# Optimization experiments

Hardware: AMD Instinct MI355X
Metric: run time of the kernel (lower is better)

Reference implementation:

```python
import jax, jax.numpy as jnp
import numpy as np

BATCH = 2048
N_MOL = 16
HEADS = 8      # C
A_DIM = 64     # embedding_dim
B_DIM = 64     # output_dim
D_IN = 64
POS_DIM = 6
CA = HEADS * A_DIM
CB = HEADS * B_DIM


def _pos_encoding(n_mol):
    # get_pos_encoding_(pos, C=6, dim_embedding=3): 3 sin + 3 cos terms
    def enc(p):
        return np.array([np.sin(p / 6.0 ** (2 * i / 3.0)) for i in (1, 2, 3)]
                        + [np.cos(p / 6.0 ** (2 * i / 3.0)) for i in (1, 2, 3)])
    return np.stack([enc(i) for i in range(n_mol)]).astype(np.float32)  # (n_mol, 6)


def setup_inputs() -> dict:
    key = jax.random.key(0)
    ks = jax.random.split(key, 8)
    d_ext = D_IN + POS_DIM

    def w(k, fi, fo):
        return jax.random.normal(k, (fi, fo), jnp.float32) / np.sqrt(fi).astype(np.float32)

    return {
        "x": jax.random.normal(ks[0], (BATCH, N_MOL, D_IN), jnp.float32),
        "flow_mask": jnp.ones((N_MOL,), jnp.float32),
        "Wk_h": w(ks[1], d_ext, CA), "bk_h": jnp.zeros((CA,), jnp.float32),
        "Wk_o": w(ks[2], CA, CA),    "bk_o": jnp.zeros((CA,), jnp.float32),
        "Wq_h": w(ks[3], d_ext, CA), "bq_h": jnp.zeros((CA,), jnp.float32),
        "Wq_o": w(ks[4], CA, CA),    "bq_o": jnp.zeros((CA,), jnp.float32),
        "Wv_h": w(ks[5], d_ext, CB), "bv_h": jnp.zeros((CB,), jnp.float32),
        "Wv_o": w(ks[6], CB, CB),    "bv_o": jnp.zeros((CB,), jnp.float32),
        "pos_emb": jnp.asarray(_pos_encoding(N_MOL)),
    }


def reference(x, flow_mask, Wk_h, bk_h, Wk_o, bk_o, Wq_h, bq_h, Wq_o, bq_o,
              Wv_h, bv_h, Wv_o, bv_o, pos_emb):
    batch = x.shape[0]
    # one_hot_extend_: append positional encoding per molecule -> (b, n_mol, d_in+6)
    xe = jnp.concatenate(
        [x, jnp.broadcast_to(pos_emb[None], (batch, N_MOL, POS_DIM))], axis=-1)

    def mlp(Wh, bh, Wo, bo):  # 1 silu hidden layer + linear output
        return jax.nn.silu(xe @ Wh + bh) @ Wo + bo

    k = mlp(Wk_h, bk_h, Wk_o, bk_o).reshape(batch, N_MOL, HEADS, A_DIM)
    q = mlp(Wq_h, bq_h, Wq_o, bq_o).reshape(batch, N_MOL, HEADS, A_DIM)
    v = mlp(Wv_h, bv_h, Wv_o, bv_o).reshape(batch, N_MOL, HEADS, B_DIM)

    norm = 1.0 / np.sqrt(A_DIM).astype(np.float32)
    # scores over molecule pairs, per head: (b, i, j, c)
    arg = jnp.einsum('i,j,bica,bjca->bijc', flow_mask, flow_mask, k, q) * norm
    w = jax.nn.softplus(arg) + 1e-5
    mask_self = 1.0 - jnp.eye(N_MOL, dtype=x.dtype)  # mask_self=True, n_mol>1
    w = w * mask_self[None, :, :, None]
    w = w / jnp.sum(w, axis=-2, keepdims=True)  # normalize over j
    # weighted combine, summing over j and heads c -> (b, n_mol, B)
    return jnp.einsum('j,bijc,bjcd->bid', flow_mask, w, v)
```

## Files before the change

### kernel.cpp

```cpp
#include <hip/hip_runtime.h>
#include <hip/hip_bf16.h>

typedef __hip_bfloat16 bf16;
typedef __attribute__((ext_vector_type(8))) short bf16x8;
typedef __attribute__((ext_vector_type(4))) float floatx4;
typedef unsigned short ushort;

#define ROWS 32768
#define KPAD 128

__global__ void prep_all(
    const float* __restrict__ x, const float* __restrict__ pos,
    const float* __restrict__ Wk_h, const float* __restrict__ Wq_h, const float* __restrict__ Wv_h,
    const float* __restrict__ Wk_o, const float* __restrict__ Wq_o, const float* __restrict__ Wv_o,
    const float* __restrict__ bk1, const float* __restrict__ bq1, const float* __restrict__ bv1,
    const float* __restrict__ bk2, const float* __restrict__ bq2, const float* __restrict__ bv2,
    bf16* __restrict__ xe, bf16* __restrict__ w1t, bf16* __restrict__ w2t,
    float* __restrict__ b1, float* __restrict__ b2)
{
  int idx = blockIdx.x * 256 + threadIdx.x;
  if (idx < 4194304) {
    int r = idx >> 7, col = idx & 127;
    float v;
    if (col < 64)      v = x[r * 64 + col];
    else if (col < 70) v = pos[(r & 15) * 6 + (col - 64)];
    else               v = 0.f;
    xe[idx] = __float2bfloat16(v);
  } else if (idx < 4194304 + 786432) {
    int i = idx - 4194304;
    int z = i >> 18, r2 = i & 262143;
    int n = r2 >> 9, k = r2 & 511;
    const float* src = (z == 0) ? Wk_o : (z == 1) ? Wq_o : Wv_o;
    w2t[i] = __float2bfloat16(src[k * 512 + n]);
  } else if (idx < 4194304 + 786432 + 196608) {
    int i = idx - 4194304 - 786432;
    int n = i >> 7, k = i & 127;
    int z = n >> 9, nl = n & 511;
    const float* src = (z == 0) ? Wk_h : (z == 1) ? Wq_h : Wv_h;
    float v = (k < 70) ? src[k * 512 + nl] : 0.f;
    w1t[i] = __float2bfloat16(v);
  } else if (idx < 4194304 + 786432 + 196608 + 3072) {
    int i = idx - 4194304 - 786432 - 196608;
    if (i < 1536) {
      int z = i >> 9, nl = i & 511;
      const float* s = (z == 0) ? bk1 : (z == 1) ? bq1 : bv1;
      b1[i] = s[nl];
    } else {
      int j = i - 1536;
      int z = j >> 9, nl = j & 511;
      const float* s = (z == 0) ? bk2 : (z == 1) ? bq2 : bv2;
      b2[j] = s[nl];
    }
  }
}

template<int SILU, int SPLITZ>
__global__ __launch_bounds__(256) void mlp_gemm(
    const bf16* __restrict__ A, int lda,
    const bf16* __restrict__ Bt, const float* __restrict__ bias,
    bf16* __restrict__ C, int ldc, int K)
{
  __shared__ __align__(16) bf16 As[128 * 32];
  __shared__ __align__(16) bf16 Bs[128 * 32];
  const int tid  = threadIdx.x;
  const int wave = tid >> 6, lane = tid & 63;

  int bnb = blockIdx.y;
  const bf16* Ap = A; const bf16* Btp = Bt; const float* biasp = bias; bf16* Cp = C;
  if (SPLITZ) {
    const int z = blockIdx.y >> 2;
    bnb = blockIdx.y & 3;
    Ap    += z * 512;
    Btp   += (long)z * 512 * K;
    biasp += z * 512;
    Cp    += (long)z * ROWS * 512;
  }
  const int bm = blockIdx.x * 128;
  const int bn = bnb * 128;
  const int wm = (wave >> 1) * 64;
  const int wn = (wave & 1) * 64;

  floatx4 acc[4][4] = {};

  const int arow = lane >> 2;
  const int acol = (lane & 3) * 8;

  for (int k0 = 0; k0 < K; k0 += 32) {
    __syncthreads();
    #pragma unroll
    for (int ch = 0; ch < 2; ++ch) {
      const int rb = wave * 32 + ch * 16;
      const bf16* ga = Ap  + (long)(bm + rb + arow) * lda + k0 + acol;
      const bf16* gb = Btp + (long)(bn + rb + arow) * K   + k0 + acol;
      __builtin_amdgcn_global_load_lds(
          (const __attribute__((address_space(1))) unsigned int*)ga,
          (__attribute__((address_space(3))) unsigned int*)(As + rb * 32), 16, 0, 0);
      __builtin_amdgcn_global_load_lds(
          (const __attribute__((address_space(1))) unsigned int*)gb,
          (__attribute__((address_space(3))) unsigned int*)(Bs + rb * 32), 16, 0, 0);
    }
    asm volatile("s_waitcnt vmcnt(0)" ::: "memory");
    __syncthreads();

    bf16x8 af[4], bfr[4];
    #pragma unroll
    for (int mi = 0; mi < 4; ++mi)
      af[mi] = *(const bf16x8*)(As + (wm + mi * 16 + (lane & 15)) * 32 + (lane >> 4) * 8);
    #pragma unroll
    for (int ni = 0; ni < 4; ++ni)
      bfr[ni] = *(const bf16x8*)(Bs + (wn + ni * 16 + (lane & 15)) * 32 + (lane >> 4) * 8);
    #pragma unroll
    for (int mi = 0; mi < 4; ++mi)
      #pragma unroll
      for (int ni = 0; ni < 4; ++ni)
        acc[mi][ni] = __builtin_amdgcn_mfma_f32_16x16x32_bf16(af[mi], bfr[ni], acc[mi][ni], 0, 0, 0);
  }

  #pragma unroll
  for (int mi = 0; mi < 4; ++mi) {
    #pragma unroll
    for (int ni = 0; ni < 4; ++ni) {
      const int nc = bn + wn + ni * 16 + (lane & 15);
      const float bv = biasp[nc];
      #pragma unroll
      for (int r = 0; r < 4; ++r) {
        const long m = bm + wm + mi * 16 + (lane >> 4) * 4 + r;
        float v = acc[mi][ni][r] + bv;
        if (SILU) v = v / (1.f + __expf(-v));
        Cp[m * (long)ldc + nc] = __float2bfloat16(v);
      }
    }
  }
}

#define ATS 520

__global__ __launch_bounds__(256) void attn_mfma(
    const bf16* __restrict__ kqv,
    const float* __restrict__ flow_mask,
    float* __restrict__ out)
{
  __shared__ ushort ks[16 * ATS];
  __shared__ ushort qs[16 * ATS];
  __shared__ ushort vs[16 * ATS];
  __shared__ ushort wn_s[4 * 16 * 40];
  __shared__ float  fm_s[16];

  const int tid  = threadIdx.x;
  const int lane = tid & 63;
  const int wave = tid >> 6;
  const int b    = blockIdx.x;
  const long rowbase = (long)b * 16 * 512;

  {
    const uint4* gk = (const uint4*)(kqv + rowbase);
    const uint4* gq = (const uint4*)(kqv + 16777216 + rowbase);
    const uint4* gv = (const uint4*)(kqv + 33554432 + rowbase);
    #pragma unroll
    for (int g = 0; g < 4; ++g) {
      const int gid = tid + g * 256;
      const int row = gid >> 6, colg = gid & 63;
      uint4 kv = gk[row * 64 + colg];
      uint4 qv = gq[row * 64 + colg];
      uint4 vv = gv[row * 64 + colg];
      *(uint4*)&ks[row * ATS + colg * 8] = kv;
      *(uint4*)&qs[row * ATS + colg * 8] = qv;
      *(uint4*)&vs[row * ATS + colg * 8] = vv;
    }
  }
  if (tid < 16) fm_s[tid] = flow_mask[tid];
  __syncthreads();

  const int jcol = lane & 15;
  const int rgrp = lane >> 4;
  const int ko   = rgrp * 8;

  {
    const float fmj = fm_s[jcol];
    #pragma unroll
    for (int h = 0; h < 2; ++h) {
      const int c = wave + h * 4;
      floatx4 acc = {};
      const ushort* kr = ks + jcol * ATS + c * 64 + ko;
      const ushort* qr = qs + jcol * ATS + c * 64 + ko;
      bf16x8 a0 = *(const bf16x8*)(kr);
      bf16x8 a1 = *(const bf16x8*)(kr + 32);
      bf16x8 b0 = *(const bf16x8*)(qr);
      bf16x8 b1 = *(const bf16x8*)(qr + 32);
      acc = __builtin_amdgcn_mfma_f32_16x16x32_bf16(a0, b0, acc, 0, 0, 0);
      acc = __builtin_amdgcn_mfma_f32_16x16x32_bf16(a1, b1, acc, 0, 0, 0);

      float w[4], s[4];
      #pragma unroll
      for (int r = 0; r < 4; ++r) {
        const int i = rgrp * 4 + r;
        float arg = acc[r] * (fm_s[i] * fmj * 0.125f);
        float sp  = fmaxf(arg, 0.f) + log1pf(__expf(-fabsf(arg)));
        float wv  = sp + 1e-5f;
        if (i == jcol) wv = 0.f;
        w[r] = wv; s[r] = wv;
      }
      #pragma unroll
      for (int m = 1; m < 16; m <<= 1) {
        #pragma unroll
        for (int r = 0; r < 4; ++r) s[r] += __shfl_xor(s[r], m);
      }
      const int hp = c >> 1, chl = c & 1;
      #pragma unroll
      for (int r = 0; r < 4; ++r) {
        const int i = rgrp * 4 + r;
        float wnv = w[r] / s[r] * fmj;
        unsigned int bi = __builtin_bit_cast(unsigned int, wnv);
        ushort bv = (ushort)((bi + 0x7fffu + ((bi >> 16) & 1u)) >> 16);
        wn_s[hp * 640 + i * 40 + chl * 16 + jcol] = bv;
      }
    }
  }
  __syncthreads();

  {
    const int dbase = wave * 16;
    const int dcol  = dbase + jcol;
    floatx4 o = {};
    #pragma unroll
    for (int hp = 0; hp < 4; ++hp) {
      bf16x8 af = *(const bf16x8*)(wn_s + hp * 640 + jcol * 40 + ko);
      const int c  = 2 * hp + (ko >> 4);
      const int jb = ko & 15;
      bf16x8 bf;
      #pragma unroll
      for (int e = 0; e < 8; ++e)
        bf[e] = (short)vs[(jb + e) * ATS + c * 64 + dcol];
      o = __builtin_amdgcn_mfma_f32_16x16x32_bf16(af, bf, o, 0, 0, 0);
    }
    float* ob = out + (long)b * 1024 + dcol;
    #pragma unroll
    for (int r = 0; r < 4; ++r) ob[(rgrp * 4 + r) * 64] = o[r];
  }
}

extern "C" void kernel_launch(void* const* d_in, const int* in_sizes, int n_in,
                              void* d_out, int out_size, void* d_ws, size_t ws_size,
                              hipStream_t stream) {
  const float* x    = (const float*)d_in[0];
  const float* fmk  = (const float*)d_in[1];
  const float* Wk_h = (const float*)d_in[2];
  const float* bk_h = (const float*)d_in[3];
  const float* Wk_o = (const float*)d_in[4];
  const float* bk_o = (const float*)d_in[5];
  const float* Wq_h = (const float*)d_in[6];
  const float* bq_h = (const float*)d_in[7];
  const float* Wq_o = (const float*)d_in[8];
  const float* bq_o = (const float*)d_in[9];
  const float* Wv_h = (const float*)d_in[10];
  const float* bv_h = (const float*)d_in[11];
  const float* Wv_o = (const float*)d_in[12];
  const float* bv_o = (const float*)d_in[13];
  const float* pos  = (const float*)d_in[14];
  float* out = (float*)d_out;

  char* ws = (char*)d_ws;
  bf16*  xe  = (bf16*)(ws + 0);
  bf16*  W1t = (bf16*)(ws + 8388608);
  bf16*  W2t = (bf16*)(ws + 8781824);
  float* b1  = (float*)(ws + 10354688);
  float* b2  = (float*)(ws + 10360832);
  const bool big = (ws_size >= 211693568ULL);

  prep_all<<<20236, 256, 0, stream>>>(x, pos, Wk_h, Wq_h, Wv_h, Wk_o, Wq_o, Wv_o,
                                      bk_h, bq_h, bv_h, bk_o, bq_o, bv_o,
                                      xe, W1t, W2t, b1, b2);

  if (big) {
    bf16* hid = (bf16*)(ws + 10366976);
    bf16* kqv = (bf16*)(ws + 111030272);
    mlp_gemm<1, 0><<<dim3(ROWS / 128, 12), 256, 0, stream>>>(
        xe, KPAD, W1t, b1, hid, 1536, KPAD);
    mlp_gemm<0, 1><<<dim3(ROWS / 128, 12), 256, 0, stream>>>(
        hid, 1536, W2t, b2, kqv, 512, 512);
    attn_mfma<<<2048, 256, 0, stream>>>(kqv, fmk, out);
  } else {
    if (ws_size < 144584704ULL) return;
    bf16* hid = (bf16*)(ws + 10366976);
    bf16* kqv = (bf16*)(ws + 43921408);
    for (int z = 0; z < 3; ++z) {
      mlp_gemm<1, 0><<<dim3(ROWS / 128, 4), 256, 0, stream>>>(
          xe, KPAD, W1t + (long)z * 512 * KPAD, b1 + z * 512, hid, 512, KPAD);
      mlp_gemm<0, 0><<<dim3(ROWS / 128, 4), 256, 0, stream>>>(
          hid, 512, W2t + (long)z * 512 * 512, b2 + z * 512,
          kqv + (long)z * ROWS * 512, 512, 512);
    }
    attn_mfma<<<2048, 256, 0, stream>>>(kqv, fmk, out);
  }
}
```

Baseline: 248.3 us.

## Fuse both MLP layers and attention into one per-block kernel

```diff
diff --git a/kernel.cpp b/kernel.cpp
--- a/kernel.cpp
+++ b/kernel.cpp
@@ -7,40 +7,35 @@
 typedef unsigned short ushort;
 
 #define ROWS 32768
-#define KPAD 128
-
-__global__ void prep_all(
-    const float* __restrict__ x, const float* __restrict__ pos,
-    const float* __restrict__ Wk_h, const float* __restrict__ Wq_h, const float* __restrict__ Wv_h,
-    const float* __restrict__ Wk_o, const float* __restrict__ Wq_o, const float* __restrict__ Wv_o,
+#define KX 96
+#define XS 104
+#define HS 520
+
+#define MFMA(a, b, c) __builtin_amdgcn_mfma_f32_16x16x32_bf16(a, b, c, 0, 0, 0)
+
+__device__ __forceinline__ ushort f2bf(float f) {
+  union { float f; unsigned int i; } u; u.f = f;
+  return (ushort)((u.i + 0x7fffu + ((u.i >> 16) & 1u)) >> 16);
+}
+__device__ __forceinline__ float b2f(ushort v) {
+  union { unsigned int i; float f; } u; u.i = (unsigned int)v << 16;
+  return u.f;
+}
+
+__global__ void prep_misc(const float* __restrict__ x, const float* __restrict__ pos,
     const float* __restrict__ bk1, const float* __restrict__ bq1, const float* __restrict__ bv1,
     const float* __restrict__ bk2, const float* __restrict__ bq2, const float* __restrict__ bv2,
-    bf16* __restrict__ xe, bf16* __restrict__ w1t, bf16* __restrict__ w2t,
-    float* __restrict__ b1, float* __restrict__ b2)
+    bf16* __restrict__ xe, float* __restrict__ b1, float* __restrict__ b2)
 {
   int idx = blockIdx.x * 256 + threadIdx.x;
-  if (idx < 4194304) {
-    int r = idx >> 7, col = idx & 127;
-    float v;
+  if (idx < ROWS * KX) {
+    int r = idx / KX, col = idx - r * KX;
+    float v = 0.f;
     if (col < 64)      v = x[r * 64 + col];
     else if (col < 70) v = pos[(r & 15) * 6 + (col - 64)];
-    else               v = 0.f;
     xe[idx] = __float2bfloat16(v);
-  } else if (idx < 4194304 + 786432) {
-    int i = idx - 4194304;
-    int z = i >> 18, r2 = i & 262143;
-    int n = r2 >> 9, k = r2 & 511;
-    const float* src = (z == 0) ? Wk_o : (z == 1) ? Wq_o : Wv_o;
-    w2t[i] = __float2bfloat16(src[k * 512 + n]);
-  } else if (idx < 4194304 + 786432 + 196608) {
-    int i = idx - 4194304 - 786432;
-    int n = i >> 7, k = i & 127;
-    int z = n >> 9, nl = n & 511;
-    const float* src = (z == 0) ? Wk_h : (z == 1) ? Wq_h : Wv_h;
-    float v = (k < 70) ? src[k * 512 + nl] : 0.f;
-    w1t[i] = __float2bfloat16(v);
-  } else if (idx < 4194304 + 786432 + 196608 + 3072) {
-    int i = idx - 4194304 - 786432 - 196608;
+  } else if (idx < ROWS * KX + 3072) {
+    int i = idx - ROWS * KX;
     if (i < 1536) {
       int z = i >> 9, nl = i & 511;
       const float* s = (z == 0) ? bk1 : (z == 1) ? bq1 : bv1;
@@ -54,188 +49,205 @@
   }
 }
 
-template<int SILU, int SPLITZ>
-__global__ __launch_bounds__(256) void mlp_gemm(
-    const bf16* __restrict__ A, int lda,
-    const bf16* __restrict__ Bt, const float* __restrict__ bias,
-    bf16* __restrict__ C, int ldc, int K)
+__global__ __launch_bounds__(256) void prep_wt(
+    const float* __restrict__ Wk_h, const float* __restrict__ Wq_h, const float* __restrict__ Wv_h,
+    const float* __restrict__ Wk_o, const float* __restrict__ Wq_o, const float* __restrict__ Wv_o,
+    bf16* __restrict__ w1t, bf16* __restrict__ w2t)
 {
-  __shared__ __align__(16) bf16 As[128 * 32];
-  __shared__ __align__(16) bf16 Bs[128 * 32];
-  const int tid  = threadIdx.x;
-  const int wave = tid >> 6, lane = tid & 63;
-
-  int bnb = blockIdx.y;
-  const bf16* Ap = A; const bf16* Btp = Bt; const float* biasp = bias; bf16* Cp = C;
-  if (SPLITZ) {
-    const int z = blockIdx.y >> 2;
-    bnb = blockIdx.y & 3;
-    Ap    += z * 512;
-    Btp   += (long)z * 512 * K;
-    biasp += z * 512;
-    Cp    += (long)z * ROWS * 512;
-  }
-  const int bm = blockIdx.x * 128;
-  const int bn = bnb * 128;
-  const int wm = (wave >> 1) * 64;
-  const int wn = (wave & 1) * 64;
-
-  floatx4 acc[4][4] = {};
-
-  const int arow = lane >> 2;
-  const int acol = (lane & 3) * 8;
-
-  for (int k0 = 0; k0 < K; k0 += 32) {
-    __syncthreads();
-    #pragma unroll
-    for (int ch = 0; ch < 2; ++ch) {
-      const int rb = wave * 32 + ch * 16;
-      const bf16* ga = Ap  + (long)(bm + rb + arow) * lda + k0 + acol;
-      const bf16* gb = Btp + (long)(bn + rb + arow) * K   + k0 + acol;
-      __builtin_amdgcn_global_load_lds(
-          (const __attribute__((address_space(1))) unsigned int*)ga,
-          (__attribute__((address_space(3))) unsigned int*)(As + rb * 32), 16, 0, 0);
-      __builtin_amdgcn_global_load_lds(
-          (const __attribute__((address_space(1))) unsigned int*)gb,
-          (__attribute__((address_space(3))) unsigned int*)(Bs + rb * 32), 16, 0, 0);
-    }
-    asm volatile("s_waitcnt vmcnt(0)" ::: "memory");
-    __syncthreads();
-
-    bf16x8 af[4], bfr[4];
-    #pragma unroll
-    for (int mi = 0; mi < 4; ++mi)
-      af[mi] = *(const bf16x8*)(As + (wm + mi * 16 + (lane & 15)) * 32 + (lane >> 4) * 8);
-    #pragma unroll
-    for (int ni = 0; ni < 4; ++ni)
-      bfr[ni] = *(const bf16x8*)(Bs + (wn + ni * 16 + (lane & 15)) * 32 + (lane >> 4) * 8);
-    #pragma unroll
-    for (int mi = 0; mi < 4; ++mi)
-      #pragma unroll
-      for (int ni = 0; ni < 4; ++ni)
-        acc[mi][ni] = __builtin_amdgcn_mfma_f32_16x16x32_bf16(af[mi], bfr[ni], acc[mi][ni], 0, 0, 0);
-  }
-
-  #pragma unroll
-  for (int mi = 0; mi < 4; ++mi) {
-    #pragma unroll
-    for (int ni = 0; ni < 4; ++ni) {
-      const int nc = bn + wn + ni * 16 + (lane & 15);
-      const float bv = biasp[nc];
-      #pragma unroll
-      for (int r = 0; r < 4; ++r) {
-        const long m = bm + wm + mi * 16 + (lane >> 4) * 4 + r;
-        float v = acc[mi][ni][r] + bv;
-        if (SILU) v = v / (1.f + __expf(-v));
-        Cp[m * (long)ldc + nc] = __float2bfloat16(v);
-      }
-    }
-  }
-}
-
-#define ATS 520
-
-__global__ __launch_bounds__(256) void attn_mfma(
-    const bf16* __restrict__ kqv,
-    const float* __restrict__ flow_mask,
+  __shared__ float tile[32][33];
+  const int bid = blockIdx.x;
+  const int c = threadIdx.x & 31, r0 = threadIdx.x >> 5;
+  if (bid < 768) {
+    const int z = bid >> 8, rem = bid & 255;
+    const int nt = rem >> 4, kt = rem & 15;
+    const float* src = (z == 0) ? Wk_o : (z == 1) ? Wq_o : Wv_o;
+    #pragma unroll
+    for (int rr = 0; rr < 4; ++rr) {
+      int r = r0 + rr * 8;
+      tile[r][c] = src[(kt * 32 + r) * 512 + nt * 32 + c];
+    }
+    __syncthreads();
+    #pragma unroll
+    for (int rr = 0; rr < 4; ++rr) {
+      int r = r0 + rr * 8;
+      w2t[((long)z * 512 + nt * 32 + r) * 512 + kt * 32 + c] = __float2bfloat16(tile[c][r]);
+    }
+  } else {
+    const int b2i = bid - 768;
+    const int z = b2i / 48, rem = b2i - z * 48;
+    const int kt = rem >> 4, nt = rem & 15;
+    const float* src = (z == 0) ? Wk_h : (z == 1) ? Wq_h : Wv_h;
+    #pragma unroll
+    for (int rr = 0; rr < 4; ++rr) {
+      int r = r0 + rr * 8;
+      int k = kt * 32 + r;
+      tile[r][c] = (k < 70) ? src[k * 512 + nt * 32 + c] : 0.f;
+    }
+    __syncthreads();
+    #pragma unroll
+    for (int rr = 0; rr < 4; ++rr) {
+      int r = r0 + rr * 8;
+      w1t[((long)z * 512 + nt * 32 + r) * KX + kt * 32 + c] = __float2bfloat16(tile[c][r]);
+    }
+  }
+}
+
+__global__ __launch_bounds__(512) void fused_all(
+    const bf16* __restrict__ xe_g, const bf16* __restrict__ w1t,
+    const bf16* __restrict__ w2t, const float* __restrict__ b1,
+    const float* __restrict__ b2, const float* __restrict__ flow_mask,
     float* __restrict__ out)
 {
-  __shared__ ushort ks[16 * ATS];
-  __shared__ ushort qs[16 * ATS];
-  __shared__ ushort vs[16 * ATS];
-  __shared__ ushort wn_s[4 * 16 * 40];
+  __shared__ ushort xe_s[32 * XS];
+  __shared__ ushort hid_s[32 * HS];
+  __shared__ ushort kq_s[2][32 * HS];
+  __shared__ ushort wn_s[2 * 4 * 16 * 40];
   __shared__ float  fm_s[16];
 
   const int tid  = threadIdx.x;
-  const int lane = tid & 63;
-  const int wave = tid >> 6;
-  const int b    = blockIdx.x;
-  const long rowbase = (long)b * 16 * 512;
+  const int w    = tid >> 6, lane = tid & 63;
+  const int jcol = lane & 15, rgrp = lane >> 4, ko = rgrp * 8;
+  const int r0   = blockIdx.x * 32;
+  const int ncol0 = w * 64;
 
   {
-    const uint4* gk = (const uint4*)(kqv + rowbase);
-    const uint4* gq = (const uint4*)(kqv + 16777216 + rowbase);
-    const uint4* gv = (const uint4*)(kqv + 33554432 + rowbase);
-    #pragma unroll
-    for (int g = 0; g < 4; ++g) {
-      const int gid = tid + g * 256;
-      const int row = gid >> 6, colg = gid & 63;
-      uint4 kv = gk[row * 64 + colg];
-      uint4 qv = gq[row * 64 + colg];
-      uint4 vv = gv[row * 64 + colg];
-      *(uint4*)&ks[row * ATS + colg * 8] = kv;
-      *(uint4*)&qs[row * ATS + colg * 8] = qv;
-      *(uint4*)&vs[row * ATS + colg * 8] = vv;
+    const int row = tid >> 4, cg = tid & 15;
+    if (cg < 12) {
+      uint4 v = *(const uint4*)(xe_g + (long)(r0 + row) * KX + cg * 8);
+      *(uint4*)&xe_s[row * XS + cg * 8] = v;
     }
   }
   if (tid < 16) fm_s[tid] = flow_mask[tid];
   __syncthreads();
 
-  const int jcol = lane & 15;
-  const int rgrp = lane >> 4;
-  const int ko   = rgrp * 8;
+  floatx4 acc[2][4];
+
+  for (int z = 0; z < 3; ++z) {
+    if (z == 2) {
+      __syncthreads();
+      const int bat = w >> 2, wv4 = w & 3;
+      const ushort* kb = kq_s[0] + bat * 16 * HS;
+      const ushort* qb = kq_s[1] + bat * 16 * HS;
+      const float fmj = fm_s[jcol];
+      #pragma unroll
+      for (int h = 0; h < 2; ++h) {
+        const int c = wv4 + h * 4;
+        floatx4 sc = {0.f, 0.f, 0.f, 0.f};
+        const ushort* kr = kb + jcol * HS + c * 64 + ko;
+        const ushort* qr = qb + jcol * HS + c * 64 + ko;
+        bf16x8 ka0 = *(const bf16x8*)kr;
+        bf16x8 ka1 = *(const bf16x8*)(kr + 32);
+        bf16x8 qa0 = *(const bf16x8*)qr;
+        bf16x8 qa1 = *(const bf16x8*)(qr + 32);
+        sc = MFMA(ka0, qa0, sc);
+        sc = MFMA(ka1, qa1, sc);
+        float wv[4], ss[4];
+        #pragma unroll
+        for (int r = 0; r < 4; ++r) {
+          const int i = rgrp * 4 + r;
+          float arg = sc[r] * (fm_s[i] * fmj * 0.125f);
+          float sp  = fmaxf(arg, 0.f) + log1pf(__expf(-fabsf(arg)));
+          float wvv = sp + 1e-5f;
+          if (i == jcol) wvv = 0.f;
+          wv[r] = wvv; ss[r] = wvv;
+        }
+        #pragma unroll
+        for (int m = 1; m < 16; m <<= 1) {
+          #pragma unroll
+          for (int r = 0; r < 4; ++r) ss[r] += __shfl_xor(ss[r], m);
+        }
+        const int hp = c >> 1, chl = c & 1;
+        #pragma unroll
+        for (int r = 0; r < 4; ++r) {
+          const int i = rgrp * 4 + r;
+          wn_s[bat * 2560 + hp * 640 + i * 40 + chl * 16 + jcol] = f2bf(wv[r] / ss[r] * fmj);
+        }
+      }
+    }
+
+    #pragma unroll
+    for (int mf = 0; mf < 2; ++mf)
+      #pragma unroll
+      for (int nf = 0; nf < 4; ++nf) acc[mf][nf] = (floatx4){0.f, 0.f, 0.f, 0.f};
+    #pragma unroll
+    for (int kk = 0; kk < 3; ++kk) {
+      const int k0 = kk * 32;
+      bf16x8 a0 = *(const bf16x8*)&xe_s[jcol * XS + k0 + ko];
+      bf16x8 a1 = *(const bf16x8*)&xe_s[(16 + jcol) * XS + k0 + ko];
+      #pragma unroll
+      for (int nf = 0; nf < 4; ++nf) {
+        const long n = (long)z * 512 + ncol0 + nf * 16 + jcol;
+        bf16x8 bfr = *(const bf16x8*)(w1t + n * KX + k0 + ko);
+        acc[0][nf] = MFMA(a0, bfr, acc[0][nf]);
+        acc[1][nf] = MFMA(a1, bfr, acc[1][nf]);
+      }
+    }
+    __syncthreads();
+    #pragma unroll
+    for (int mf = 0; mf < 2; ++mf)
+      #pragma unroll
+      for (int nf = 0; nf < 4; ++nf) {
+        const int col = ncol0 + nf * 16 + jcol;
+        const float bv = b1[z * 512 + col];
+        #pragma unroll
+        for (int r = 0; r < 4; ++r) {
+          float v = acc[mf][nf][r] + bv;
+          v = v / (1.f + __expf(-v));
+          hid_s[(mf * 16 + rgrp * 4 + r) * HS + col] = f2bf(v);
+        }
+      }
+    __syncthreads();
+
+    #pragma unroll
+    for (int mf = 0; mf < 2; ++mf)
+      #pragma unroll
+      for (int nf = 0; nf < 4; ++nf) acc[mf][nf] = (floatx4){0.f, 0.f, 0.f, 0.f};
+    #pragma unroll 4
+    for (int kk = 0; kk < 16; ++kk) {
+      const int k0 = kk * 32;
+      bf16x8 a0 = *(const bf16x8*)&hid_s[jcol * HS + k0 + ko];
+      bf16x8 a1 = *(const bf16x8*)&hid_s[(16 + jcol) * HS + k0 + ko];
+      #pragma unroll
+      for (int nf = 0; nf < 4; ++nf) {
+        const long n = (long)z * 512 + ncol0 + nf * 16 + jcol;
+        bf16x8 bfr = *(const bf16x8*)(w2t + n * 512 + k0 + ko);
+        acc[0][nf] = MFMA(a0, bfr, acc[0][nf]);
+        acc[1][nf] = MFMA(a1, bfr, acc[1][nf]);
+      }
+    }
+    ushort* dst = (z == 1) ? kq_s[1] : kq_s[0];
+    #pragma unroll
+    for (int mf = 0; mf < 2; ++mf)
+      #pragma unroll
+      for (int nf = 0; nf < 4; ++nf) {
+        const int col = ncol0 + nf * 16 + jcol;
+        const float bv = b2[z * 512 + col];
+        #pragma unroll
+        for (int r = 0; r < 4; ++r)
+          dst[(mf * 16 + rgrp * 4 + r) * HS + col] = f2bf(acc[mf][nf][r] + bv);
+      }
+  }
+  __syncthreads();
 
   {
-    const float fmj = fm_s[jcol];
-    #pragma unroll
-    for (int h = 0; h < 2; ++h) {
-      const int c = wave + h * 4;
-      floatx4 acc = {};
-      const ushort* kr = ks + jcol * ATS + c * 64 + ko;
-      const ushort* qr = qs + jcol * ATS + c * 64 + ko;
-      bf16x8 a0 = *(const bf16x8*)(kr);
-      bf16x8 a1 = *(const bf16x8*)(kr + 32);
-      bf16x8 b0 = *(const bf16x8*)(qr);
-      bf16x8 b1 = *(const bf16x8*)(qr + 32);
-      acc = __builtin_amdgcn_mfma_f32_16x16x32_bf16(a0, b0, acc, 0, 0, 0);
-      acc = __builtin_amdgcn_mfma_f32_16x16x32_bf16(a1, b1, acc, 0, 0, 0);
-
-      float w[4], s[4];
-      #pragma unroll
-      for (int r = 0; r < 4; ++r) {
-        const int i = rgrp * 4 + r;
-        float arg = acc[r] * (fm_s[i] * fmj * 0.125f);
-        float sp  = fmaxf(arg, 0.f) + log1pf(__expf(-fabsf(arg)));
-        float wv  = sp + 1e-5f;
-        if (i == jcol) wv = 0.f;
-        w[r] = wv; s[r] = wv;
-      }
-      #pragma unroll
-      for (int m = 1; m < 16; m <<= 1) {
-        #pragma unroll
-        for (int r = 0; r < 4; ++r) s[r] += __shfl_xor(s[r], m);
-      }
-      const int hp = c >> 1, chl = c & 1;
-      #pragma unroll
-      for (int r = 0; r < 4; ++r) {
-        const int i = rgrp * 4 + r;
-        float wnv = w[r] / s[r] * fmj;
-        unsigned int bi = __builtin_bit_cast(unsigned int, wnv);
-        ushort bv = (ushort)((bi + 0x7fffu + ((bi >> 16) & 1u)) >> 16);
-        wn_s[hp * 640 + i * 40 + chl * 16 + jcol] = bv;
-      }
-    }
-  }
-  __syncthreads();
-
-  {
-    const int dbase = wave * 16;
-    const int dcol  = dbase + jcol;
-    floatx4 o = {};
+    const int bat  = w >> 2;
+    const int dcol = (w & 3) * 16 + jcol;
+    floatx4 o = {0.f, 0.f, 0.f, 0.f};
     #pragma unroll
     for (int hp = 0; hp < 4; ++hp) {
-      bf16x8 af = *(const bf16x8*)(wn_s + hp * 640 + jcol * 40 + ko);
+      bf16x8 af = *(const bf16x8*)&wn_s[bat * 2560 + hp * 640 + jcol * 40 + ko];
       const int c  = 2 * hp + (ko >> 4);
       const int jb = ko & 15;
-      bf16x8 bf;
+      bf16x8 bfr;
       #pragma unroll
       for (int e = 0; e < 8; ++e)
-        bf[e] = (short)vs[(jb + e) * ATS + c * 64 + dcol];
-      o = __builtin_amdgcn_mfma_f32_16x16x32_bf16(af, bf, o, 0, 0, 0);
-    }
-    float* ob = out + (long)b * 1024 + dcol;
-    #pragma unroll
-    for (int r = 0; r < 4; ++r) ob[(rgrp * 4 + r) * 64] = o[r];
+        bfr[e] = (short)kq_s[0][(bat * 16 + jb + e) * HS + c * 64 + dcol];
+      o = MFMA(af, bfr, o);
+    }
+    const long gb = (long)blockIdx.x * 2 + bat;
+    #pragma unroll
+    for (int r = 0; r < 4; ++r)
+      out[gb * 1024 + (rgrp * 4 + r) * 64 + dcol] = o[r];
   }
 }
 
@@ -261,35 +273,14 @@
 
   char* ws = (char*)d_ws;
   bf16*  xe  = (bf16*)(ws + 0);
-  bf16*  W1t = (bf16*)(ws + 8388608);
-  bf16*  W2t = (bf16*)(ws + 8781824);
-  float* b1  = (float*)(ws + 10354688);
-  float* b2  = (float*)(ws + 10360832);
-  const bool big = (ws_size >= 211693568ULL);
-
-  prep_all<<<20236, 256, 0, stream>>>(x, pos, Wk_h, Wq_h, Wv_h, Wk_o, Wq_o, Wv_o,
-                                      bk_h, bq_h, bv_h, bk_o, bq_o, bv_o,
-                                      xe, W1t, W2t, b1, b2);
-
-  if (big) {
-    bf16* hid = (bf16*)(ws + 10366976);
-    bf16* kqv = (bf16*)(ws + 111030272);
-    mlp_gemm<1, 0><<<dim3(ROWS / 128, 12), 256, 0, stream>>>(
-        xe, KPAD, W1t, b1, hid, 1536, KPAD);
-    mlp_gemm<0, 1><<<dim3(ROWS / 128, 12), 256, 0, stream>>>(
-        hid, 1536, W2t, b2, kqv, 512, 512);
-    attn_mfma<<<2048, 256, 0, stream>>>(kqv, fmk, out);
-  } else {
-    if (ws_size < 144584704ULL) return;
-    bf16* hid = (bf16*)(ws + 10366976);
-    bf16* kqv = (bf16*)(ws + 43921408);
-    for (int z = 0; z < 3; ++z) {
-      mlp_gemm<1, 0><<<dim3(ROWS / 128, 4), 256, 0, stream>>>(
-          xe, KPAD, W1t + (long)z * 512 * KPAD, b1 + z * 512, hid, 512, KPAD);
-      mlp_gemm<0, 0><<<dim3(ROWS / 128, 4), 256, 0, stream>>>(
-          hid, 512, W2t + (long)z * 512 * 512, b2 + z * 512,
-          kqv + (long)z * ROWS * 512, 512, 512);
-    }
-    attn_mfma<<<2048, 256, 0, stream>>>(kqv, fmk, out);
-  }
-}
+  bf16*  w1t = (bf16*)(ws + 6291456);
+  bf16*  w2t = (bf16*)(ws + 6586368);
+  float* b1  = (float*)(ws + 8159232);
+  float* b2  = (float*)(ws + 8165376);
+  if (ws_size < 8171520ULL) return;
+
+  prep_misc<<<12300, 256, 0, stream>>>(x, pos, bk_h, bq_h, bv_h, bk_o, bq_o, bv_o,
+                                       xe, b1, b2);
+  prep_wt<<<912, 256, 0, stream>>>(Wk_h, Wq_h, Wv_h, Wk_o, Wq_o, Wv_o, w1t, w2t);
+  fused_all<<<1024, 512, 0, stream>>>(xe, w1t, w2t, b1, b2, fmk, out);
+}
```

Measured after the change: 337.8 us. 1.36x slower.
